# Optimization experiments

Hardware: AMD Instinct MI355X
Metric: run time of the kernel (lower is better)

The kernel has to match this reference:

```python
import jax, jax.numpy as jnp
import numpy as np

B, T, IN, H, OUT = 512, 1000, 39, 64, 48


def setup_inputs() -> dict:
    key = jax.random.key(0)
    ks = jax.random.split(key, 7)
    s = 1.0 / np.sqrt(H)
    return {
        "x": jax.random.normal(ks[0], (B, T, IN), dtype=jnp.float32),
        "W_ih": jax.random.uniform(ks[1], (4 * H, IN), minval=-s, maxval=s, dtype=jnp.float32),
        "W_hh": jax.random.uniform(ks[2], (4 * H, H), minval=-s, maxval=s, dtype=jnp.float32),
        "b_ih": jax.random.uniform(ks[3], (4 * H,), minval=-s, maxval=s, dtype=jnp.float32),
        "b_hh": jax.random.uniform(ks[4], (4 * H,), minval=-s, maxval=s, dtype=jnp.float32),
        "W_out": jax.random.uniform(ks[5], (OUT, H), minval=-s, maxval=s, dtype=jnp.float32),
        "b_out": jax.random.uniform(ks[6], (OUT,), minval=-s, maxval=s, dtype=jnp.float32),
    }


def reference(x, W_ih, W_hh, b_ih, b_hh, W_out, b_out):
    # Single-layer batch-first LSTM (zero init state) + per-step Linear + sigmoid.
    b = b_ih + b_hh  # [4H]
    # Precompute input projections for all timesteps at once: [T, B, 4H]
    xg = jnp.einsum('bti,gi->tbg', x, W_ih) + b

    def step(carry, xg_t):
        h, c = carry
        gates = xg_t + h @ W_hh.T  # [B, 4H], gate order i, f, g, o
        i, f, g, o = jnp.split(gates, 4, axis=-1)
        c = jax.nn.sigmoid(f) * c + jax.nn.sigmoid(i) * jnp.tanh(g)
        h = jax.nn.sigmoid(o) * jnp.tanh(c)
        y = jax.nn.sigmoid(h @ W_out.T + b_out)  # [B, OUT]
        return (h, c), y

    h0 = jnp.zeros((x.shape[0], W_hh.shape[1]), dtype=x.dtype)
    (_, _), ys = jax.lax.scan(step, (h0, h0), xg)  # ys: [T, B, OUT]
    return jnp.swapaxes(ys, 0, 1)  # [B, T, OUT]
```

## Files before the change

### kernel.cpp

```cpp
#include <hip/hip_runtime.h>


#define BB 512
#define TT 1000
#define INF 39
#define HH 64
#define OUTF 48
#define G4 (4 * HH)

typedef float v2f __attribute__((ext_vector_type(2)));

#define Q10(M) M(0) M(1) M(2) M(3) M(4) M(5) M(6) M(7) M(8) M(9)
#define Q16(M) M(0) M(1) M(2) M(3) M(4) M(5) M(6) M(7) \
               M(8) M(9) M(10) M(11) M(12) M(13) M(14) M(15)

__global__ __launch_bounds__(256)
__attribute__((amdgpu_waves_per_eu(2, 2)))
void lstm_fused_kernel(
    const float* __restrict__ x,
    const float* __restrict__ W_ih,
    const float* __restrict__ W_hh,
    const float* __restrict__ b_ih,
    const float* __restrict__ b_hh,
    const float* __restrict__ W_out,
    const float* __restrict__ b_out,
    float* __restrict__ out)
{
    const int b = blockIdx.x;
    const int tid = threadIdx.x;

    __shared__ float xs[40];
    __shared__ float hs[HH];
    __shared__ float act[G4];

    const float* wih_ptr = W_ih + tid * INF;
#define LOAD_IH4(q) v2f wiA##q, wiB##q; \
    wiA##q.x = wih_ptr[4*(q)]; \
    wiA##q.y = (4*(q)+1 < INF) ? wih_ptr[4*(q)+1] : 0.f; \
    wiB##q.x = (4*(q)+2 < INF) ? wih_ptr[4*(q)+2] : 0.f; \
    wiB##q.y = (4*(q)+3 < INF) ? wih_ptr[4*(q)+3] : 0.f; \
    asm volatile("" : "+v"(wiA##q), "+v"(wiB##q));
    Q10(LOAD_IH4)

    const float4* wh4p = (const float4*)(W_hh + tid * HH);
#define LOAD_HH4(i) const float4 whq##i = wh4p[i]; \
    v2f whA##i = {whq##i.x, whq##i.y}; \
    v2f whB##i = {whq##i.z, whq##i.w}; \
    asm volatile("" : "+v"(whA##i), "+v"(whB##i));
    Q16(LOAD_HH4)

    float bias = b_ih[tid] + b_hh[tid];
    asm volatile("" : "+v"(bias));

    const int o = tid >> 2;
    const int p = tid & 3;
    v2f woA0, woB0, woA1, woB1, woA2, woB2, woA3, woB3;
    float bo = 0.f;
    if (tid < 4 * OUTF) {
        const float4* wop = (const float4*)(W_out + o * HH + p * 16);
        const float4 q0 = wop[0], q1 = wop[1], q2 = wop[2], q3 = wop[3];
        woA0 = (v2f){q0.x, q0.y}; woB0 = (v2f){q0.z, q0.w};
        woA1 = (v2f){q1.x, q1.y}; woB1 = (v2f){q1.z, q1.w};
        woA2 = (v2f){q2.x, q2.y}; woB2 = (v2f){q2.z, q2.w};
        woA3 = (v2f){q3.x, q3.y}; woB3 = (v2f){q3.z, q3.w};
        bo = b_out[o];
    } else {
        woA0 = woB0 = woA1 = woB1 = (v2f){0.f, 0.f};
        woA2 = woB2 = woA3 = woB3 = (v2f){0.f, 0.f};
    }
    asm volatile("" : "+v"(woA0), "+v"(woB0), "+v"(woA1), "+v"(woB1),
                     "+v"(woA2), "+v"(woB2), "+v"(woA3), "+v"(woB3), "+v"(bo));

    float c = 0.f;
    const size_t x_base = (size_t)b * TT * INF;
    const size_t out_base = (size_t)b * TT * OUTF;

    if (tid < HH) hs[tid] = 0.f;
    if (tid < INF) xs[tid] = x[x_base + tid];
    if (tid == 39) xs[39] = 0.f;
    float xreg = (tid < INF) ? x[x_base + INF + tid] : 0.f;

    const int gate_type = tid >> 6;
    __syncthreads();

    const float4* xs4 = (const float4*)xs;
    const float4* hs4 = (const float4*)hs;

    for (int t = 0; t < TT; ++t) {
        v2f accA = {bias, 0.f};
        v2f accB = {0.f, 0.f};
#define FMA_IH4(q) { const float4 xv = xs4[q]; \
        const v2f xA = {xv.x, xv.y}; const v2f xB = {xv.z, xv.w}; \
        accA += xA * wiA##q; accB += xB * wiB##q; }
        Q10(FMA_IH4)
#define FMA_HH4(i) { const float4 hv = hs4[i]; \
        const v2f hA = {hv.x, hv.y}; const v2f hB = {hv.z, hv.w}; \
        accA += hA * whA##i; accB += hB * whB##i; }
        Q16(FMA_HH4)
        const float acc = (accA.x + accA.y) + (accB.x + accB.y);

        float a;
        if (gate_type == 2) {
            a = 2.f / (1.f + __expf(-2.f * acc)) - 1.f;
        } else {
            a = 1.f / (1.f + __expf(-acc));
        }
        act[tid] = a;
        __syncthreads();

        if (tid < INF) {
            xs[tid] = xreg;
            if (t + 2 < TT) xreg = x[x_base + (size_t)(t + 2) * INF + tid];
        }
        if (tid < HH) {
            const float ig = act[tid];
            const float fg = act[HH + tid];
            const float gg = act[2 * HH + tid];
            const float og = act[3 * HH + tid];
            c = fg * c + ig * gg;
            const float th = 2.f / (1.f + __expf(-2.f * c)) - 1.f;
            hs[tid] = og * th;
        }
        __syncthreads();

        if (tid < 4 * OUTF) {
            const float4 h0 = hs4[p * 4 + 0];
            const float4 h1 = hs4[p * 4 + 1];
            const float4 h2 = hs4[p * 4 + 2];
            const float4 h3 = hs4[p * 4 + 3];
            v2f sA = {0.f, 0.f}, sB = {0.f, 0.f};
            { const v2f a2 = {h0.x, h0.y}; const v2f b2 = {h0.z, h0.w};
              sA += a2 * woA0; sB += b2 * woB0; }
            { const v2f a2 = {h1.x, h1.y}; const v2f b2 = {h1.z, h1.w};
              sA += a2 * woA1; sB += b2 * woB1; }
            { const v2f a2 = {h2.x, h2.y}; const v2f b2 = {h2.z, h2.w};
              sA += a2 * woA2; sB += b2 * woB2; }
            { const v2f a2 = {h3.x, h3.y}; const v2f b2 = {h3.z, h3.w};
              sA += a2 * woA3; sB += b2 * woB3; }
            float s = (sA.x + sA.y) + (sB.x + sB.y);
            s += __shfl_xor(s, 1, 64);
            s += __shfl_xor(s, 2, 64);
            if (p == 0) {
                const float y = 1.f / (1.f + __expf(-(s + bo)));
                __builtin_nontemporal_store(y, &out[out_base + (size_t)t * OUTF + o]);
            }
        }
    }
}

extern "C" void kernel_launch(void* const* d_in, const int* in_sizes, int n_in,
                              void* d_out, int out_size, void* d_ws, size_t ws_size,
                              hipStream_t stream) {
    const float* x     = (const float*)d_in[0];
    const float* W_ih  = (const float*)d_in[1];
    const float* W_hh  = (const float*)d_in[2];
    const float* b_ih  = (const float*)d_in[3];
    const float* b_hh  = (const float*)d_in[4];
    const float* W_out = (const float*)d_in[5];
    const float* b_out = (const float*)d_in[6];
    float* out = (float*)d_out;

    lstm_fused_kernel<<<dim3(BB), dim3(G4), 0, stream>>>(
        x, W_ih, W_hh, b_ih, b_hh, W_out, b_out, out);
}
```

Baseline: 1.033 ms.

## Broadcast hidden state via readlane and split waves across LSTM roles

Each lane now loads one element of h from LDS, and the recurrent matvec broadcasts it through scalar readlane instead of every thread reading float4 vectors of h from shared memory. The x staging moves to wave 1 and the output projection to waves 1-3, so the cell update on wave 0 runs concurrently with the x prefetch rather than sharing the same wave. The recurrent FMAs switch from packed v2f ops to scalar fmaf with four accumulators. This is meant to cut LDS bandwidth and latency on the serial step, but 64 readlanes per step add SALU work and scalar-to-vector dependencies.

```diff
diff --git a/kernel.cpp b/kernel.cpp
--- a/kernel.cpp
+++ b/kernel.cpp
@@ -14,8 +14,8 @@
 #define Q16(M) M(0) M(1) M(2) M(3) M(4) M(5) M(6) M(7) \
                M(8) M(9) M(10) M(11) M(12) M(13) M(14) M(15)
 
-__global__ __launch_bounds__(256)
-__attribute__((amdgpu_waves_per_eu(2, 2)))
+__global__ __attribute__((amdgpu_flat_work_group_size(256, 256),
+                          amdgpu_waves_per_eu(2, 2)))
 void lstm_fused_kernel(
     const float* __restrict__ x,
     const float* __restrict__ W_ih,
@@ -28,6 +28,8 @@
 {
     const int b = blockIdx.x;
     const int tid = threadIdx.x;
+    const int lane = tid & 63;
+    const int wav = tid >> 6;
 
     __shared__ float xs[40];
     __shared__ float hs[HH];
@@ -39,24 +41,27 @@
     wiA##q.y = (4*(q)+1 < INF) ? wih_ptr[4*(q)+1] : 0.f; \
     wiB##q.x = (4*(q)+2 < INF) ? wih_ptr[4*(q)+2] : 0.f; \
     wiB##q.y = (4*(q)+3 < INF) ? wih_ptr[4*(q)+3] : 0.f; \
-    asm volatile("" : "+v"(wiA##q), "+v"(wiB##q));
+    asm volatile("" : "+v"(wiA##q)); \
+    asm volatile("" : "+v"(wiB##q));
     Q10(LOAD_IH4)
 
     const float4* wh4p = (const float4*)(W_hh + tid * HH);
 #define LOAD_HH4(i) const float4 whq##i = wh4p[i]; \
     v2f whA##i = {whq##i.x, whq##i.y}; \
     v2f whB##i = {whq##i.z, whq##i.w}; \
-    asm volatile("" : "+v"(whA##i), "+v"(whB##i));
+    asm volatile("" : "+v"(whA##i)); \
+    asm volatile("" : "+v"(whB##i));
     Q16(LOAD_HH4)
 
     float bias = b_ih[tid] + b_hh[tid];
     asm volatile("" : "+v"(bias));
 
-    const int o = tid >> 2;
-    const int p = tid & 3;
+    const int ot = tid - 64;
+    const int o = ot >> 2;
+    const int p = ot & 3;
     v2f woA0, woB0, woA1, woB1, woA2, woB2, woA3, woB3;
     float bo = 0.f;
-    if (tid < 4 * OUTF) {
+    if (tid >= 64) {
         const float4* wop = (const float4*)(W_out + o * HH + p * 16);
         const float4 q0 = wop[0], q1 = wop[1], q2 = wop[2], q3 = wop[3];
         woA0 = (v2f){q0.x, q0.y}; woB0 = (v2f){q0.z, q0.w};
@@ -68,39 +73,53 @@
         woA0 = woB0 = woA1 = woB1 = (v2f){0.f, 0.f};
         woA2 = woB2 = woA3 = woB3 = (v2f){0.f, 0.f};
     }
-    asm volatile("" : "+v"(woA0), "+v"(woB0), "+v"(woA1), "+v"(woB1),
-                     "+v"(woA2), "+v"(woB2), "+v"(woA3), "+v"(woB3), "+v"(bo));
+    asm volatile("" : "+v"(woA0)); asm volatile("" : "+v"(woB0));
+    asm volatile("" : "+v"(woA1)); asm volatile("" : "+v"(woB1));
+    asm volatile("" : "+v"(woA2)); asm volatile("" : "+v"(woB2));
+    asm volatile("" : "+v"(woA3)); asm volatile("" : "+v"(woB3));
+    asm volatile("" : "+v"(bo));
 
     float c = 0.f;
     const size_t x_base = (size_t)b * TT * INF;
     const size_t out_base = (size_t)b * TT * OUTF;
 
     if (tid < HH) hs[tid] = 0.f;
-    if (tid < INF) xs[tid] = x[x_base + tid];
-    if (tid == 39) xs[39] = 0.f;
-    float xreg = (tid < INF) ? x[x_base + INF + tid] : 0.f;
+    if (wav == 1 && lane < INF) xs[lane] = x[x_base + lane];
+    if (wav == 1 && lane == INF) xs[INF] = 0.f;
+    float xreg = (wav == 1 && lane < INF) ? x[x_base + INF + lane] : 0.f;
 
-    const int gate_type = tid >> 6;
     __syncthreads();
 
     const float4* xs4 = (const float4*)xs;
     const float4* hs4 = (const float4*)hs;
 
     for (int t = 0; t < TT; ++t) {
-        v2f accA = {bias, 0.f};
-        v2f accB = {0.f, 0.f};
+        v2f xaA = {bias, 0.f};
+        v2f xaB = {0.f, 0.f};
 #define FMA_IH4(q) { const float4 xv = xs4[q]; \
         const v2f xA = {xv.x, xv.y}; const v2f xB = {xv.z, xv.w}; \
-        accA += xA * wiA##q; accB += xB * wiB##q; }
+        xaA += xA * wiA##q; xaB += xB * wiB##q; }
         Q10(FMA_IH4)
-#define FMA_HH4(i) { const float4 hv = hs4[i]; \
-        const v2f hA = {hv.x, hv.y}; const v2f hB = {hv.z, hv.w}; \
-        accA += hA * whA##i; accB += hB * whB##i; }
-        Q16(FMA_HH4)
-        const float acc = (accA.x + accA.y) + (accB.x + accB.y);
+
+        const float hval = hs[lane];
+        const int hbits = __float_as_int(hval);
+        float a0 = 0.f, a1 = 0.f, a2 = 0.f, a3 = 0.f;
+#define RLF(j) __int_as_float(__builtin_amdgcn_readlane(hbits, (j)))
+#define FMA_HH4(i, J) { \
+        a0 = fmaf(RLF((J) + 0), whA##i.x, a0); \
+        a1 = fmaf(RLF((J) + 1), whA##i.y, a1); \
+        a2 = fmaf(RLF((J) + 2), whB##i.x, a2); \
+        a3 = fmaf(RLF((J) + 3), whB##i.y, a3); }
+        FMA_HH4(0, 0)   FMA_HH4(1, 4)   FMA_HH4(2, 8)   FMA_HH4(3, 12)
+        FMA_HH4(4, 16)  FMA_HH4(5, 20)  FMA_HH4(6, 24)  FMA_HH4(7, 28)
+        FMA_HH4(8, 32)  FMA_HH4(9, 36)  FMA_HH4(10, 40) FMA_HH4(11, 44)
+        FMA_HH4(12, 48) FMA_HH4(13, 52) FMA_HH4(14, 56) FMA_HH4(15, 60)
+
+        const float acc = ((xaA.x + xaA.y) + (xaB.x + xaB.y))
+                        + ((a0 + a1) + (a2 + a3));
 
         float a;
-        if (gate_type == 2) {
+        if (wav == 2) {
             a = 2.f / (1.f + __expf(-2.f * acc)) - 1.f;
         } else {
             a = 1.f / (1.f + __expf(-acc));
@@ -108,22 +127,23 @@
         act[tid] = a;
         __syncthreads();
 
-        if (tid < INF) {
-            xs[tid] = xreg;
-            if (t + 2 < TT) xreg = x[x_base + (size_t)(t + 2) * INF + tid];
-        }
-        if (tid < HH) {
-            const float ig = act[tid];
-            const float fg = act[HH + tid];
-            const float gg = act[2 * HH + tid];
-            const float og = act[3 * HH + tid];
+        if (wav == 1) {
+            if (lane < INF) {
+                xs[lane] = xreg;
+                if (t + 2 < TT) xreg = x[x_base + (size_t)(t + 2) * INF + lane];
+            }
+        } else if (wav == 0) {
+            const float ig = act[lane];
+            const float fg = act[HH + lane];
+            const float gg = act[2 * HH + lane];
+            const float og = act[3 * HH + lane];
             c = fg * c + ig * gg;
             const float th = 2.f / (1.f + __expf(-2.f * c)) - 1.f;
-            hs[tid] = og * th;
+            hs[lane] = og * th;
         }
         __syncthreads();
 
-        if (tid < 4 * OUTF) {
+        if (tid >= 64) {
             const float4 h0 = hs4[p * 4 + 0];
             const float4 h1 = hs4[p * 4 + 1];
             const float4 h2 = hs4[p * 4 + 2];
```

New measurement: 1.248 ms. 20.8% more time.
